# Kernel tuning notes

Hardware: AMD Instinct MI355X
Metric: run time of the kernel (lower is better)

The kernel has to match this reference:

```python
import jax, jax.numpy as jnp
import numpy as np

N_NODES = 100000
N_EDGES = 600000
N_ETYPES = 3
N_LAYERS = 3  # n_layers + 1 conv layers
D = 128
EPS = 1e-5


def setup_inputs() -> dict:
    key = jax.random.key(0)
    ks = jax.random.split(key, 8)
    scale = 1.0 / np.sqrt(D)
    x = jax.random.normal(ks[0], (N_NODES, D), dtype=jnp.float32)
    src = jax.random.randint(ks[1], (N_ETYPES, N_EDGES), 0, N_NODES, dtype=jnp.int32)
    dst = jax.random.randint(ks[2], (N_ETYPES, N_EDGES), 0, N_NODES, dtype=jnp.int32)
    W_self = jax.random.normal(ks[3], (N_LAYERS, N_ETYPES, D, D), dtype=jnp.float32) * scale
    W_neigh = jax.random.normal(ks[4], (N_LAYERS, N_ETYPES, D, D), dtype=jnp.float32) * scale
    b = jax.random.normal(ks[5], (N_LAYERS, N_ETYPES, D), dtype=jnp.float32) * 0.01
    gamma = jnp.ones((N_LAYERS, D), dtype=jnp.float32)
    beta = jnp.zeros((N_LAYERS, D), dtype=jnp.float32)
    return {"x": x, "src": src, "dst": dst, "W_self": W_self, "W_neigh": W_neigh,
            "b": b, "gamma": gamma, "beta": beta}


def reference(x, src, dst, W_self, W_neigh, b, gamma, beta):
    N = x.shape[0]
    L, K = W_self.shape[0], W_self.shape[1]
    # in-degree per etype (DGL mean aggregator: zero-degree -> 0 neighbor feat)
    degs = [jnp.clip(jax.ops.segment_sum(jnp.ones((dst.shape[1],), x.dtype), dst[k],
                                         num_segments=N), 1.0, None)
            for k in range(K)]
    h = x
    for l in range(L):
        acc = jnp.zeros((N, W_self.shape[-1]), x.dtype)
        for k in range(K):
            # gather src feats, mean-aggregate onto dst: [N, D]
            neigh = jax.ops.segment_sum(h[src[k]], dst[k], num_segments=N) / degs[k][:, None]
            o = h @ W_self[l, k] + neigh @ W_neigh[l, k] + b[l, k]
            if l < L - 1:  # activation inside SAGEConv, last layer has none
                o = jax.nn.relu(o)
            acc = acc + o  # HeteroGraphConv aggregate='sum'
        # BatchNorm1d, training mode (biased batch variance)
        mu = acc.mean(axis=0)
        var = ((acc - mu) ** 2).mean(axis=0)
        h = gamma[l] * (acc - mu) / jnp.sqrt(var + EPS) + beta[l]
    return h
```

## Files before the change

### kernel.cpp

```cpp
#include <hip/hip_runtime.h>

#define NN 100000
#define NNP 100096
#define NE 600000
#define KE 3
#define NL 3
#define D  128
#define EPS 1e-5f
#define NB 391
#define NBKT 196
#define EPB 4096
#define NEB 147
#define NSL 16

typedef __attribute__((ext_vector_type(8))) short short8;
typedef __attribute__((ext_vector_type(4))) float floatx4;

__device__ __forceinline__ void atomic_add_f32(float* p, float v) { unsafeAtomicAdd(p, v); }

__device__ __forceinline__ float bf2f(unsigned int u16) {
    unsigned int v = u16 << 16;
    return __builtin_bit_cast(float, v);
}
__device__ __forceinline__ unsigned int f2bf(float f) {
    unsigned int u = __builtin_bit_cast(unsigned int, f);
    u += 0x7FFFu + ((u >> 16) & 1u);
    return u >> 16;
}
__device__ __forceinline__ unsigned int pack2(float a, float b) {
    return f2bf(a) | (f2bf(b) << 16);
}

__device__ __forceinline__ void gload16(const void* g, void* l) {
    __builtin_amdgcn_global_load_lds(
        (const __attribute__((address_space(1))) void*)g,
        (__attribute__((address_space(3))) void*)l, 16, 0, 0);
}

__global__ void convert_x_kernel(const float* __restrict__ x, ushort* __restrict__ hbf) {
    size_t i = (size_t)blockIdx.x * blockDim.x + threadIdx.x;
    if (i >= (size_t)NN * D / 4) return;
    float4 v = *(const float4*)(x + i * 4);
    uint2 o;
    o.x = pack2(v.x, v.y);
    o.y = pack2(v.z, v.w);
    *(uint2*)(hbf + i * 4) = o;
}

__global__ void wprep_kernel(const float* __restrict__ Ws, const float* __restrict__ Wn,
                             ushort* __restrict__ Bt) {
    int idx = blockIdx.x * blockDim.x + threadIdx.x;
    if (idx >= NL * KE * 128 * 256) return;
    int lk  = idx >> 15;
    int rem = idx & 32767;
    int n   = rem >> 8;
    int kk  = rem & 255;
    float v = (kk < 128) ? Ws[(size_t)lk * 16384 + kk * 128 + n]
                         : Wn[(size_t)lk * 16384 + (kk - 128) * 128 + n];
    Bt[idx] = (ushort)f2bf(v);
}

__global__ void fold_kernel(const float* __restrict__ Wsl, const float* __restrict__ bsrc,
                            const float* __restrict__ ssl, ushort* __restrict__ Btl,
                            float* __restrict__ biasW) {
    const int k = blockIdx.x;
    const int n = threadIdx.x;
    const float* W = Wsl + (size_t)k * D * D;
    ushort* B = Btl + (size_t)k * 32768;
    float acc = 0.f;
    #pragma unroll 4
    for (int kk = 0; kk < D; ++kk) {
        float w = W[kk * D + n];
        acc += ssl[D + kk] * w;
        B[n * 256 + kk] = (ushort)f2bf(ssl[kk] * w);
    }
    biasW[k * D + n] = bsrc[k * D + n] + acc;
}

__global__ void bucket_count_kernel(const int* __restrict__ dst,
                                    int* __restrict__ bucketTotal, int* __restrict__ blockBase) {
    const int blk = blockIdx.x;
    const int k = blk / NEB, cb = blk - k * NEB;
    __shared__ int hist[NBKT];
    for (int i = threadIdx.x; i < NBKT; i += 256) hist[i] = 0;
    __syncthreads();
    const int e0 = cb * EPB, e1 = min(e0 + EPB, NE);
    for (int e = e0 + threadIdx.x; e < e1; e += 256)
        atomicAdd(&hist[dst[(size_t)k * NE + e] >> 9], 1);
    __syncthreads();
    for (int i = threadIdx.x; i < NBKT; i += 256) {
        int c = hist[i];
        int base = c ? atomicAdd(&bucketTotal[k * NBKT + i], c) : 0;
        blockBase[(size_t)blk * NBKT + i] = base;
    }
}

__global__ void bucket_scan_kernel(const int* __restrict__ bucketTotal,
                                   int* __restrict__ bucketStart) {
    __shared__ int sd[1024];
    const int t = threadIdx.x;
    int v = (t < KE * NBKT) ? bucketTotal[t] : 0;
    sd[t] = v;
    __syncthreads();
    for (int off = 1; off < 1024; off <<= 1) {
        int u = (t >= off) ? sd[t - off] : 0;
        __syncthreads();
        sd[t] += u;
        __syncthreads();
    }
    if (t < KE * NBKT) bucketStart[t] = sd[t] - v;
}

__global__ void bucket_scatter_kernel(const int* __restrict__ src, const int* __restrict__ dst,
                                      const int* __restrict__ bucketStart,
                                      const int* __restrict__ blockBase,
                                      uint2* __restrict__ ebuf) {
    const int blk = blockIdx.x;
    const int k = blk / NEB, cb = blk - k * NEB;
    __shared__ int hist[NBKT], binoff[NBKT], cur[NBKT];
    __shared__ int sc[256];
    __shared__ uint2 stage[EPB];
    const int t = threadIdx.x;
    for (int i = t; i < NBKT; i += 256) hist[i] = 0;
    __syncthreads();
    const int e0 = cb * EPB, e1 = min(e0 + EPB, NE);
    for (int e = e0 + t; e < e1; e += 256)
        atomicAdd(&hist[dst[(size_t)k * NE + e] >> 9], 1);
    __syncthreads();
    int hv = (t < NBKT) ? hist[t] : 0;
    sc[t] = hv;
    __syncthreads();
    for (int off = 1; off < 256; off <<= 1) {
        int u = (t >= off) ? sc[t - off] : 0;
        __syncthreads();
        sc[t] += u;
        __syncthreads();
    }
    if (t < NBKT) { binoff[t] = sc[t] - hv; cur[t] = sc[t] - hv; }
    __syncthreads();
    for (int e = e0 + t; e < e1; e += 256) {
        int d = dst[(size_t)k * NE + e], s = src[(size_t)k * NE + e];
        int b = d >> 9;
        int p = atomicAdd(&cur[b], 1);
        stage[p] = make_uint2((unsigned)s, (unsigned)d);
    }
    __syncthreads();
    const int n = e1 - e0;
    for (int i = t; i < n; i += 256) {
        uint2 ed = stage[i];
        int b = (int)(ed.y >> 9);
        int pos = bucketStart[k * NBKT + b] + blockBase[(size_t)blk * NBKT + b] + (i - binoff[b]);
        ebuf[pos] = ed;
    }
}

__global__ void bucket_deg_kernel(const uint2* __restrict__ ebuf,
                                  const int* __restrict__ bucketStart, int* __restrict__ degi) {
    const int blk = blockIdx.x;
    const int k = blk / NBKT, b = blk - k * NBKT;
    __shared__ int cnt[512];
    for (int i = threadIdx.x; i < 512; i += 256) cnt[i] = 0;
    __syncthreads();
    const int s0 = bucketStart[blk];
    const int s1 = (blk + 1 < KE * NBKT) ? bucketStart[blk + 1] : KE * NE;
    for (int e = s0 + threadIdx.x; e < s1; e += 256)
        atomicAdd(&cnt[ebuf[e].y & 511], 1);
    __syncthreads();
    const int n0 = b << 9;
    for (int i = threadIdx.x; i < 512; i += 256) {
        int node = n0 + i;
        if (node < NN) degi[(size_t)k * NN + node] = cnt[i];
    }
}

__global__ void scan_a_kernel(const int* __restrict__ degi, int* __restrict__ bsum) {
    const int b = blockIdx.x;
    const int k = b / NB, lb = b - k * NB;
    const int t = threadIdx.x;
    const int i = lb * 256 + t;
    int deg = (i < NN) ? degi[(size_t)k * NN + i] : 0;
    __shared__ int sd[256];
    sd[t] = deg;
    __syncthreads();
    for (int off = 128; off > 0; off >>= 1) {
        if (t < off) sd[t] += sd[t + off];
        __syncthreads();
    }
    if (t == 0) bsum[b] = sd[0];
}

__global__ void scan_b_kernel(int* __restrict__ bsum) {
    const int k = blockIdx.x;
    const int t = threadIdx.x;
    int v = (t < NB) ? bsum[k * NB + t] : 0;
    __shared__ int sd[512];
    sd[t] = v;
    __syncthreads();
    for (int off = 1; off < 512; off <<= 1) {
        int u = (t >= off) ? sd[t - off] : 0;
        __syncthreads();
        sd[t] += u;
        __syncthreads();
    }
    if (t < NB) bsum[k * NB + t] = sd[t] - v;
}

__global__ void scan_c_kernel(const int* __restrict__ degi, const int* __restrict__ bsum,
                              int* __restrict__ rowptr, float* __restrict__ invdeg) {
    const int b = blockIdx.x;
    const int k = b / NB, lb = b - k * NB;
    const int t = threadIdx.x;
    const int i = lb * 256 + t;
    int deg = (i < NN) ? degi[(size_t)k * NN + i] : 0;
    __shared__ int sd[256];
    sd[t] = deg;
    __syncthreads();
    for (int off = 1; off < 256; off <<= 1) {
        int u = (t >= off) ? sd[t - off] : 0;
        __syncthreads();
        sd[t] += u;
        __syncthreads();
    }
    int val = bsum[b] + sd[t] - deg;
    if (i < NN) {
        rowptr[(size_t)k * (NN + 1) + i] = val;
        invdeg[(size_t)k * NN + i] = 1.0f / (float)max(deg, 1);
    }
    if (i == NN) rowptr[(size_t)k * (NN + 1) + NN] = NE;
}

__global__ void bucket_fill_kernel(const uint2* __restrict__ ebuf,
                                   const int* __restrict__ bucketStart,
                                   const int* __restrict__ rowptr, int* __restrict__ csr) {
    const int blk = blockIdx.x;
    const int k = blk / NBKT, b = blk - k * NBKT;
    __shared__ int cur[512];
    const int n0 = b << 9;
    for (int i = threadIdx.x; i < 512; i += 256) {
        int node = n0 + i;
        cur[i] = (node < NN) ? rowptr[(size_t)k * (NN + 1) + node] : 0;
    }
    __syncthreads();
    const int s0 = bucketStart[blk];
    const int s1 = (blk + 1 < KE * NBKT) ? bucketStart[blk + 1] : KE * NE;
    for (int e = s0 + threadIdx.x; e < s1; e += 256) {
        uint2 ed = ebuf[e];
        int p = atomicAdd(&cur[ed.y & 511], 1);
        csr[(size_t)k * NE + p] = (int)ed.x;
    }
}

__global__ void gather3_kernel(const ushort* __restrict__ hsrc, const int* __restrict__ csr,
                               const int* __restrict__ rowptr, const float* __restrict__ invdeg,
                               ushort* __restrict__ neigh, const float* __restrict__ ssl,
                               int affine) {
    int g = blockIdx.x * 16 + (threadIdx.x >> 4);
    if (g >= KE * NN) return;
    int k = g / NN, node = g - k * NN;
    const int q = (threadIdx.x & 15) * 8;
    const int* rp = rowptr + (size_t)k * (NN + 1) + node;
    const int* cs = csr + (size_t)k * NE;
    int beg = rp[0], end = rp[1];
    float f0=0,f1=0,f2=0,f3=0,f4=0,f5=0,f6=0,f7=0;
    int j = beg;
    for (; j + 4 <= end; j += 4) {
        int s0 = cs[j], s1 = cs[j + 1], s2 = cs[j + 2], s3 = cs[j + 3];
        uint4 a = *(const uint4*)(hsrc + (size_t)s0 * D + q);
        uint4 b = *(const uint4*)(hsrc + (size_t)s1 * D + q);
        uint4 c = *(const uint4*)(hsrc + (size_t)s2 * D + q);
        uint4 d = *(const uint4*)(hsrc + (size_t)s3 * D + q);
        f0 += bf2f(a.x & 0xffff) + bf2f(b.x & 0xffff) + bf2f(c.x & 0xffff) + bf2f(d.x & 0xffff);
        f1 += bf2f(a.x >> 16)    + bf2f(b.x >> 16)    + bf2f(c.x >> 16)    + bf2f(d.x >> 16);
        f2 += bf2f(a.y & 0xffff) + bf2f(b.y & 0xffff) + bf2f(c.y & 0xffff) + bf2f(d.y & 0xffff);
        f3 += bf2f(a.y >> 16)    + bf2f(b.y >> 16)    + bf2f(c.y >> 16)    + bf2f(d.y >> 16);
        f4 += bf2f(a.z & 0xffff) + bf2f(b.z & 0xffff) + bf2f(c.z & 0xffff) + bf2f(d.z & 0xffff);
        f5 += bf2f(a.z >> 16)    + bf2f(b.z >> 16)    + bf2f(c.z >> 16)    + bf2f(d.z >> 16);
        f6 += bf2f(a.w & 0xffff) + bf2f(b.w & 0xffff) + bf2f(c.w & 0xffff) + bf2f(d.w & 0xffff);
        f7 += bf2f(a.w >> 16)    + bf2f(b.w >> 16)    + bf2f(c.w >> 16)    + bf2f(d.w >> 16);
    }
    for (; j < end; ++j) {
        int s0 = cs[j];
        uint4 a = *(const uint4*)(hsrc + (size_t)s0 * D + q);
        f0 += bf2f(a.x & 0xffff); f1 += bf2f(a.x >> 16);
        f2 += bf2f(a.y & 0xffff); f3 += bf2f(a.y >> 16);
        f4 += bf2f(a.z & 0xffff); f5 += bf2f(a.z >> 16);
        f6 += bf2f(a.w & 0xffff); f7 += bf2f(a.w >> 16);
    }
    float iv = invdeg[g];
    float r0 = f0 * iv, r1 = f1 * iv, r2 = f2 * iv, r3 = f3 * iv;
    float r4 = f4 * iv, r5 = f5 * iv, r6 = f6 * iv, r7 = f7 * iv;
    if (affine) {
        float4 c0 = *(const float4*)(ssl + q);
        float4 c1 = *(const float4*)(ssl + q + 4);
        float4 h0 = *(const float4*)(ssl + D + q);
        float4 h1 = *(const float4*)(ssl + D + q + 4);
        float m = (end > beg) ? 1.0f : 0.0f;
        r0 = r0 * c0.x + m * h0.x;  r1 = r1 * c0.y + m * h0.y;
        r2 = r2 * c0.z + m * h0.z;  r3 = r3 * c0.w + m * h0.w;
        r4 = r4 * c1.x + m * h1.x;  r5 = r5 * c1.y + m * h1.y;
        r6 = r6 * c1.z + m * h1.z;  r7 = r7 * c1.w + m * h1.w;
    }
    uint4 o;
    o.x = pack2(r0, r1);
    o.y = pack2(r2, r3);
    o.z = pack2(r4, r5);
    o.w = pack2(r6, r7);
    *(uint4*)(neigh + (size_t)k * NNP * D + (size_t)node * D + q) = o;
}

__global__ __launch_bounds__(512, 4)
void layer_gemm_kernel(const ushort* __restrict__ hself, const ushort* __restrict__ neigh,
                       const ushort* __restrict__ Bt,
                       const float* __restrict__ bias,
                       ushort* __restrict__ accb, int relu,
                       float* __restrict__ colsum, float* __restrict__ colsq) {
    __shared__ __align__(16) ushort Asf[2][128][64];
    __shared__ __align__(16) ushort Anb[2][128][64];
    __shared__ __align__(16) ushort Bst[128][64];
    const int tid  = threadIdx.x;
    const int wave = tid >> 6, lane = tid & 63;
    const int wm = wave & 1, wn = wave >> 1;
    const int lrow = lane & 15, quad = lane >> 4;
    const int m0 = blockIdx.x * 128;
    const int srow  = lane >> 3;
    const int scolb = ((lane & 7) ^ srow) << 4;

    {
        const char* Ab = (const char*)hself + (size_t)m0 * 256;
        #pragma unroll
        for (int kc = 0; kc < 2; ++kc)
            #pragma unroll
            for (int i = 0; i < 2; ++i)
                gload16(Ab + (size_t)(wave * 16 + i * 8 + srow) * 256 + kc * 128 + scolb,
                        (char*)Asf + kc * 16384 + wave * 2048 + i * 1024);
    }

    floatx4 tot[4][2];
    #pragma unroll
    for (int a = 0; a < 4; ++a)
        #pragma unroll
        for (int b = 0; b < 2; ++b)
            tot[a][b] = (floatx4){0.f, 0.f, 0.f, 0.f};

    for (int k = 0; k < KE; ++k) {
        const char* Btk = (const char*)Bt + (size_t)k * 65536;
        __syncthreads();
        {
            const char* Ab = (const char*)(neigh + (size_t)k * NNP * D) + (size_t)m0 * 256;
            #pragma unroll
            for (int kc = 0; kc < 2; ++kc)
                #pragma unroll
                for (int i = 0; i < 2; ++i)
                    gload16(Ab + (size_t)(wave * 16 + i * 8 + srow) * 256 + kc * 128 + scolb,
                            (char*)Anb + kc * 16384 + wave * 2048 + i * 1024);
        }
        #pragma unroll
        for (int i = 0; i < 2; ++i)
            gload16(Btk + (size_t)(wave * 16 + i * 8 + srow) * 512 + scolb,
                    (char*)Bst + wave * 2048 + i * 1024);

        floatx4 o4[4][2];
        #pragma unroll
        for (int a = 0; a < 4; ++a)
            #pragma unroll
            for (int b = 0; b < 2; ++b)
                o4[a][b] = (floatx4){0.f, 0.f, 0.f, 0.f};
        #pragma unroll
        for (int idx = 0; idx < 4; ++idx) {
            __syncthreads();
            const char* Ab = (idx >> 1) ? (const char*)Anb : (const char*)Asf;
            const int kcoff = (idx & 1) * 16384;
            #pragma unroll
            for (int ks = 0; ks < 2; ++ks) {
                short8 af[4], bfr[2];
                const int cb = ks * 64 + quad * 16;
                #pragma unroll
                for (int im = 0; im < 4; ++im) {
                    int ra = wm * 64 + im * 16 + lrow;
                    af[im] = *(const short8*)(Ab + kcoff + ra * 128 + (cb ^ ((ra & 7) << 4)));
                }
                #pragma unroll
                for (int in = 0; in < 2; ++in) {
                    int rb = wn * 32 + in * 16 + lrow;
                    bfr[in] = *(const short8*)((const char*)Bst + rb * 128 + (cb ^ ((rb & 7) << 4)));
                }
                #pragma unroll
                for (int im = 0; im < 4; ++im)
                    #pragma unroll
                    for (int in = 0; in < 2; ++in)
                        o4[im][in] = __builtin_amdgcn_mfma_f32_16x16x32_bf16(
                            af[im], bfr[in], o4[im][in], 0, 0, 0);
            }
            if (idx < 3) {
                __syncthreads();
                const int p2 = (idx + 1) >> 1, k2 = (idx + 1) & 1;
                #pragma unroll
                for (int i = 0; i < 2; ++i)
                    gload16(Btk + (size_t)(wave * 16 + i * 8 + srow) * 512 + p2 * 256 + k2 * 128 + scolb,
                            (char*)Bst + wave * 2048 + i * 1024);
            }
        }
        const float* bk = bias + k * D;
        float bv[2];
        #pragma unroll
        for (int in = 0; in < 2; ++in) bv[in] = bk[wn * 32 + in * 16 + lrow];
        #pragma unroll
        for (int im = 0; im < 4; ++im)
            #pragma unroll
            for (int in = 0; in < 2; ++in)
                #pragma unroll
                for (int r = 0; r < 4; ++r) {
                    float v = o4[im][in][r] + bv[in];
                    if (relu) v = fmaxf(v, 0.f);
                    tot[im][in][r] += v;
                }
    }

    float ls[2] = {0.f, 0.f}, lq[2] = {0.f, 0.f};
    #pragma unroll
    for (int im = 0; im < 4; ++im)
        #pragma unroll
        for (int r = 0; r < 4; ++r) {
            int row = m0 + wm * 64 + im * 16 + quad * 4 + r;
            bool ok = row < NN;
            #pragma unroll
            for (int in = 0; in < 2; ++in) {
                float v = ok ? tot[im][in][r] : 0.f;
                ls[in] += v;
                lq[in] += v * v;
            }
        }
    __syncthreads();
    float* redS = (float*)&Anb[0][0][0];
    float* redQ = redS + 1024;
    #pragma unroll
    for (int in = 0; in < 2; ++in) {
        int col = wn * 32 + in * 16 + lrow;
        int slot = col * 8 + wm * 4 + quad;
        redS[slot] = ls[in];
        redQ[slot] = lq[in];
    }
    __syncthreads();
    if (tid < 128) {
        float s = 0.f, q = 0.f;
        #pragma unroll
        for (int i = 0; i < 8; ++i) { s += redS[tid * 8 + i]; q += redQ[tid * 8 + i]; }
        int slice = blockIdx.x & (NSL - 1);
        atomic_add_f32(&colsum[slice * D + tid], s);
        atomic_add_f32(&colsq[slice * D + tid], q);
    }

    ushort* Cs = &Asf[0][0][0];
    #pragma unroll
    for (int im = 0; im < 4; ++im)
        #pragma unroll
        for (int r = 0; r < 4; ++r) {
            int rl = wm * 64 + im * 16 + quad * 4 + r;
            #pragma unroll
            for (int in = 0; in < 2; ++in)
                Cs[rl * 128 + wn * 32 + in * 16 + lrow] = (ushort)f2bf(tot[im][in][r]);
        }
    __syncthreads();
    #pragma unroll
    for (int jj = 0; jj < 4; ++jj) {
        int c8 = tid + jj * 512;
        int rl = c8 >> 4;
        int cc = (c8 & 15) * 8;
        int row = m0 + rl;
        if (row < NN)
            *(uint4*)(accb + (size_t)row * D + cc) = *(const uint4*)(Cs + rl * 128 + cc);
    }
}

__global__ void finalize_kernel(const float* __restrict__ colsum, const float* __restrict__ colsq,
                                const float* __restrict__ gamma, const float* __restrict__ beta,
                                float* __restrict__ ssl) {
    int c = threadIdx.x;
    float s = 0.f, q = 0.f;
    #pragma unroll
    for (int i = 0; i < NSL; ++i) { s += colsum[i * D + c]; q += colsq[i * D + c]; }
    float mu  = s * (1.0f / NN);
    float var = q * (1.0f / NN) - mu * mu;
    float sc  = gamma[c] * rsqrtf(var + EPS);
    ssl[c]     = sc;
    ssl[D + c] = beta[c] - mu * sc;
}

__global__ void bn_kernel(const ushort* __restrict__ accb, const float* __restrict__ ssl,
                          float* __restrict__ out) {
    size_t i = (size_t)blockIdx.x * blockDim.x + threadIdx.x;
    if (i >= (size_t)NN * D / 4) return;
    int c4 = (int)(i & 31) << 2;
    uint2 a = *(const uint2*)(accb + i * 4);
    float4 v = {bf2f(a.x & 0xffff), bf2f(a.x >> 16), bf2f(a.y & 0xffff), bf2f(a.y >> 16)};
    float4 sc = *(const float4*)(ssl + c4);
    float4 sh = *(const float4*)(ssl + D + c4);
    float4 o;
    o.x = v.x * sc.x + sh.x;
    o.y = v.y * sc.y + sh.y;
    o.z = v.z * sc.z + sh.z;
    o.w = v.w * sc.w + sh.w;
    *(float4*)(out + i * 4) = o;
}

extern "C" void kernel_launch(void* const* d_in, const int* in_sizes, int n_in,
                              void* d_out, int out_size, void* d_ws, size_t ws_size,
                              hipStream_t stream) {
    const float* x       = (const float*)d_in[0];
    const int*   src     = (const int*)d_in[1];
    const int*   dst     = (const int*)d_in[2];
    const float* W_self  = (const float*)d_in[3];
    const float* W_neigh = (const float*)d_in[4];
    const float* bvec    = (const float*)d_in[5];
    const float* gamma   = (const float*)d_in[6];
    const float* beta    = (const float*)d_in[7];
    float* out = (float*)d_out;

    ushort* accb   = (ushort*)d_ws;
    float*  invdeg = (float*)(accb + (size_t)NNP * D);
    float*  colsum = invdeg + (size_t)KE * NN;
    float*  colsq  = colsum + NL * NSL * D;
    float*  ss     = colsq + NL * NSL * D;
    float*  biasW  = ss + NL * 2 * D;
    ushort* hbf    = (ushort*)(biasW + KE * D);
    ushort* neigh  = hbf + (size_t)NNP * D;
    ushort* Btw    = neigh + (size_t)KE * NNP * D;
    int*    degi   = (int*)(Btw + (size_t)NL * KE * 128 * 256);
    int*    rowptr = degi + (size_t)KE * NN;
    int*    csr    = rowptr + (size_t)KE * (NN + 1);
    int*    bsum   = csr + (size_t)KE * NE;
    int*    bucketTotal = bsum + (size_t)KE * NB;
    int*    bucketStart = bucketTotal + KE * NBKT;
    int*    blockBase   = bucketStart + KE * NBKT;
    uint2*  ebuf   = (uint2*)accb;

    convert_x_kernel<<<(int)(((size_t)NN * D / 4 + 255) / 256), 256, 0, stream>>>(x, hbf);
    wprep_kernel<<<(NL * KE * 128 * 256 + 255) / 256, 256, 0, stream>>>(W_self, W_neigh, Btw);
    hipMemsetAsync(colsum, 0, sizeof(float) * 2 * NL * NSL * D, stream);

    hipMemsetAsync(bucketTotal, 0, sizeof(int) * KE * NBKT, stream);
    bucket_count_kernel<<<KE * NEB, 256, 0, stream>>>(dst, bucketTotal, blockBase);
    bucket_scan_kernel<<<1, 1024, 0, stream>>>(bucketTotal, bucketStart);
    bucket_scatter_kernel<<<KE * NEB, 256, 0, stream>>>(src, dst, bucketStart, blockBase, ebuf);
    bucket_deg_kernel<<<KE * NBKT, 256, 0, stream>>>(ebuf, bucketStart, degi);
    scan_a_kernel<<<KE * NB, 256, 0, stream>>>(degi, bsum);
    scan_b_kernel<<<KE, 512, 0, stream>>>(bsum);
    scan_c_kernel<<<KE * NB, 256, 0, stream>>>(degi, bsum, rowptr, invdeg);
    bucket_fill_kernel<<<KE * NBKT, 256, 0, stream>>>(ebuf, bucketStart, rowptr, csr);

    for (int l = 0; l < NL; ++l) {
        int relu = (l < NL - 1) ? 1 : 0;
        const ushort* hsrc = (l == 0) ? hbf : accb;
        const float*  ssl  = ss + (size_t)(l ? l - 1 : 0) * 2 * D;
        gather3_kernel<<<(KE * NN + 15) / 16, 256, 0, stream>>>(
            hsrc, csr, rowptr, invdeg, neigh, ssl, l > 0);
        layer_gemm_kernel<<<NNP / 128, 512, 0, stream>>>(
            hsrc, neigh,
            Btw + (size_t)l * KE * 128 * 256,
            (l == 0) ? bvec : biasW,
            accb, relu,
            colsum + (size_t)l * NSL * D, colsq + (size_t)l * NSL * D);
        finalize_kernel<<<1, 128, 0, stream>>>(
            colsum + (size_t)l * NSL * D, colsq + (size_t)l * NSL * D,
            gamma + (size_t)l * D, beta + (size_t)l * D, ss + (size_t)l * 2 * D);
        if (l + 1 < NL)
            fold_kernel<<<KE, 128, 0, stream>>>(
                W_self + (size_t)(l + 1) * KE * D * D,
                bvec + (size_t)(l + 1) * KE * D,
                ss + (size_t)l * 2 * D,
                Btw + (size_t)(l + 1) * KE * 128 * 256,
                biasW);
    }
    bn_kernel<<<(int)(((size_t)NN * D / 4 + 255) / 256), 256, 0, stream>>>(
        accb, ss + (size_t)(NL - 1) * 2 * D, out);
}
```

Baseline: 572.1 us.

## Double-buffer A and B tiles across a flattened 12-stage GEMM loop

Restructures the per-layer GEMM so each of the 12 K-chunks (3 etypes x 4 chunks, self and neighbor halves) stages both its A and B 64-column slices into a double-buffered shared array. The next chunk's loads are issued before the current chunk's MFMAs run. The hself tile is no longer kept resident; it is reloaded for each etype. This aims to overlap global-to-LDS transfer with compute and cut the extra barriers. It does add redundant reads of hself and B, though shared memory use drops from 80KB to 64KB, which may allow higher occupancy.

```diff
diff --git a/kernel.cpp b/kernel.cpp
--- a/kernel.cpp
+++ b/kernel.cpp
@@ -314,9 +314,7 @@
                        const float* __restrict__ bias,
                        ushort* __restrict__ accb, int relu,
                        float* __restrict__ colsum, float* __restrict__ colsq) {
-    __shared__ __align__(16) ushort Asf[2][128][64];
-    __shared__ __align__(16) ushort Anb[2][128][64];
-    __shared__ __align__(16) ushort Bst[128][64];
+    __shared__ __align__(16) ushort ST[2][2][128][64];
     const int tid  = threadIdx.x;
     const int wave = tid >> 6, lane = tid & 63;
     const int wm = wave & 1, wn = wave >> 1;
@@ -325,96 +323,89 @@
     const int srow  = lane >> 3;
     const int scolb = ((lane & 7) ^ srow) << 4;
 
-    {
-        const char* Ab = (const char*)hself + (size_t)m0 * 256;
-        #pragma unroll
-        for (int kc = 0; kc < 2; ++kc)
-            #pragma unroll
-            for (int i = 0; i < 2; ++i)
-                gload16(Ab + (size_t)(wave * 16 + i * 8 + srow) * 256 + kc * 128 + scolb,
-                        (char*)Asf + kc * 16384 + wave * 2048 + i * 1024);
-    }
-
-    floatx4 tot[4][2];
+#define STAGE(b, kk, cc)                                                                 \
+    {                                                                                    \
+        const char* Asrc = ((cc) < 2) ? (const char*)hself                               \
+                                      : (const char*)(neigh + (size_t)(kk) * NNP * D);   \
+        const char* Bsrc = (const char*)Bt + (size_t)(kk) * 65536;                       \
+        char* Adst = (char*)&ST[b][0][0][0];                                             \
+        char* Bdst = (char*)&ST[b][1][0][0];                                             \
+        _Pragma("unroll")                                                                \
+        for (int i = 0; i < 2; ++i) {                                                    \
+            int r = wave * 16 + i * 8 + srow;                                            \
+            gload16(Asrc + (size_t)(m0 + r) * 256 + ((cc) & 1) * 128 + scolb,            \
+                    Adst + wave * 2048 + i * 1024);                                      \
+        }                                                                                \
+        _Pragma("unroll")                                                                \
+        for (int i = 0; i < 2; ++i) {                                                    \
+            int n = wave * 16 + i * 8 + srow;                                            \
+            gload16(Bsrc + (size_t)n * 512 + (cc) * 128 + scolb,                         \
+                    Bdst + wave * 2048 + i * 1024);                                      \
+        }                                                                                \
+    }
+
+    floatx4 tot[4][2], o4[4][2];
     #pragma unroll
     for (int a = 0; a < 4; ++a)
         #pragma unroll
-        for (int b = 0; b < 2; ++b)
+        for (int b = 0; b < 2; ++b) {
             tot[a][b] = (floatx4){0.f, 0.f, 0.f, 0.f};
-
-    for (int k = 0; k < KE; ++k) {
-        const char* Btk = (const char*)Bt + (size_t)k * 65536;
-        __syncthreads();
-        {
-            const char* Ab = (const char*)(neigh + (size_t)k * NNP * D) + (size_t)m0 * 256;
-            #pragma unroll
-            for (int kc = 0; kc < 2; ++kc)
+            o4[a][b]  = (floatx4){0.f, 0.f, 0.f, 0.f};
+        }
+
+    STAGE(0, 0, 0);
+
+    int cur = 0;
+    #pragma unroll
+    for (int p = 0; p < 4 * KE; ++p) {
+        __syncthreads();
+        if (p + 1 < 4 * KE) {
+            const int pn = p + 1;
+            STAGE(cur ^ 1, pn >> 2, pn & 3);
+        }
+        const char* Ab = (const char*)&ST[cur][0][0][0];
+        const char* Bb = (const char*)&ST[cur][1][0][0];
+        #pragma unroll
+        for (int ks = 0; ks < 2; ++ks) {
+            short8 af[4], bfr[2];
+            const int cb = ks * 64 + quad * 16;
+            #pragma unroll
+            for (int im = 0; im < 4; ++im) {
+                int ra = wm * 64 + im * 16 + lrow;
+                af[im] = *(const short8*)(Ab + ra * 128 + (cb ^ ((ra & 7) << 4)));
+            }
+            #pragma unroll
+            for (int in = 0; in < 2; ++in) {
+                int rb = wn * 32 + in * 16 + lrow;
+                bfr[in] = *(const short8*)(Bb + rb * 128 + (cb ^ ((rb & 7) << 4)));
+            }
+            #pragma unroll
+            for (int im = 0; im < 4; ++im)
                 #pragma unroll
-                for (int i = 0; i < 2; ++i)
-                    gload16(Ab + (size_t)(wave * 16 + i * 8 + srow) * 256 + kc * 128 + scolb,
-                            (char*)Anb + kc * 16384 + wave * 2048 + i * 1024);
+                for (int in = 0; in < 2; ++in)
+                    o4[im][in] = __builtin_amdgcn_mfma_f32_16x16x32_bf16(
+                        af[im], bfr[in], o4[im][in], 0, 0, 0);
         }
-        #pragma unroll
-        for (int i = 0; i < 2; ++i)
-            gload16(Btk + (size_t)(wave * 16 + i * 8 + srow) * 512 + scolb,
-                    (char*)Bst + wave * 2048 + i * 1024);
-
-        floatx4 o4[4][2];
-        #pragma unroll
-        for (int a = 0; a < 4; ++a)
-            #pragma unroll
-            for (int b = 0; b < 2; ++b)
-                o4[a][b] = (floatx4){0.f, 0.f, 0.f, 0.f};
-        #pragma unroll
-        for (int idx = 0; idx < 4; ++idx) {
-            __syncthreads();
-            const char* Ab = (idx >> 1) ? (const char*)Anb : (const char*)Asf;
-            const int kcoff = (idx & 1) * 16384;
-            #pragma unroll
-            for (int ks = 0; ks < 2; ++ks) {
-                short8 af[4], bfr[2];
-                const int cb = ks * 64 + quad * 16;
+        if ((p & 3) == 3) {
+            const float* bk = bias + (p >> 2) * D;
+            float bv[2];
+            #pragma unroll
+            for (int in = 0; in < 2; ++in) bv[in] = bk[wn * 32 + in * 16 + lrow];
+            #pragma unroll
+            for (int im = 0; im < 4; ++im)
                 #pragma unroll
-                for (int im = 0; im < 4; ++im) {
-                    int ra = wm * 64 + im * 16 + lrow;
-                    af[im] = *(const short8*)(Ab + kcoff + ra * 128 + (cb ^ ((ra & 7) << 4)));
-                }
-                #pragma unroll
-                for (int in = 0; in < 2; ++in) {
-                    int rb = wn * 32 + in * 16 + lrow;
-                    bfr[in] = *(const short8*)((const char*)Bst + rb * 128 + (cb ^ ((rb & 7) << 4)));
-                }
-                #pragma unroll
-                for (int im = 0; im < 4; ++im)
+                for (int in = 0; in < 2; ++in)
                     #pragma unroll
-                    for (int in = 0; in < 2; ++in)
-                        o4[im][in] = __builtin_amdgcn_mfma_f32_16x16x32_bf16(
-                            af[im], bfr[in], o4[im][in], 0, 0, 0);
-            }
-            if (idx < 3) {
-                __syncthreads();
-                const int p2 = (idx + 1) >> 1, k2 = (idx + 1) & 1;
-                #pragma unroll
-                for (int i = 0; i < 2; ++i)
-                    gload16(Btk + (size_t)(wave * 16 + i * 8 + srow) * 512 + p2 * 256 + k2 * 128 + scolb,
-                            (char*)Bst + wave * 2048 + i * 1024);
-            }
+                    for (int r = 0; r < 4; ++r) {
+                        float v = o4[im][in][r] + bv[in];
+                        if (relu) v = fmaxf(v, 0.f);
+                        tot[im][in][r] += v;
+                        o4[im][in][r] = 0.f;
+                    }
         }
-        const float* bk = bias + k * D;
-        float bv[2];
-        #pragma unroll
-        for (int in = 0; in < 2; ++in) bv[in] = bk[wn * 32 + in * 16 + lrow];
-        #pragma unroll
-        for (int im = 0; im < 4; ++im)
-            #pragma unroll
-            for (int in = 0; in < 2; ++in)
-                #pragma unroll
-                for (int r = 0; r < 4; ++r) {
-                    float v = o4[im][in][r] + bv[in];
-                    if (relu) v = fmaxf(v, 0.f);
-                    tot[im][in][r] += v;
-                }
-    }
+        cur ^= 1;
+    }
+#undef STAGE
 
     float ls[2] = {0.f, 0.f}, lq[2] = {0.f, 0.f};
     #pragma unroll
@@ -431,7 +422,7 @@
             }
         }
     __syncthreads();
-    float* redS = (float*)&Anb[0][0][0];
+    float* redS = (float*)&ST[1][0][0][0];
     float* redQ = redS + 1024;
     #pragma unroll
     for (int in = 0; in < 2; ++in) {
@@ -450,7 +441,7 @@
         atomic_add_f32(&colsq[slice * D + tid], q);
     }
 
-    ushort* Cs = &Asf[0][0][0];
+    ushort* Cs = &ST[0][0][0][0];
     #pragma unroll
     for (int im = 0; im < 4; ++im)
         #pragma unroll
```

New measurement: 553.9 us. 3.2% less time.
